# Kernel tuning notes

Hardware: AMD Instinct MI355X
Metric: run time of the kernel (lower is better)

## Reference

```python
import jax, jax.numpy as jnp
import numpy as np
import math

# Config (matches init_kwargs)
V, D, L, H, KVH, FF = 4054, 1024, 8, 16, 8, 4096
HD = D // H            # 64
NREP = H // KVH        # 2
THETA = 500000.0
EPS = 1e-5
PAD = 4053
B, S = 2, 2048


def setup_inputs() -> dict:
    key = jax.random.key(0)
    ks = jax.random.split(key, 12)
    std = 0.02
    inp = {
        "input_ids": jax.random.randint(ks[0], (B, S), 0, 4050),
        "emb": jax.random.normal(ks[1], (V, D), jnp.float32) * std,
        # Linear weights stored as [in, out] so y = x @ W
        "Wq": jax.random.normal(ks[2], (L, D, H * HD), jnp.float32) * std,
        "Wk": jax.random.normal(ks[3], (L, D, KVH * HD), jnp.float32) * std,
        "Wv": jax.random.normal(ks[4], (L, D, KVH * HD), jnp.float32) * std,
        "Wo": jax.random.normal(ks[5], (L, H * HD, D), jnp.float32) * std,
        "Wg": jax.random.normal(ks[6], (L, D, FF), jnp.float32) * std,
        "Wu": jax.random.normal(ks[7], (L, D, FF), jnp.float32) * std,
        "Wd": jax.random.normal(ks[8], (L, FF, D), jnp.float32) * std,
        "attn_norm_w": jnp.ones((L, D), jnp.float32),
        "ffn_norm_w": jnp.ones((L, D), jnp.float32),
        "final_norm_w": jnp.ones((D,), jnp.float32),
        "lm_head": jax.random.normal(ks[9], (D, V), jnp.float32) * std,
    }
    return inp


def _rms_norm(x, w):
    return x * jax.lax.rsqrt(jnp.mean(x * x, axis=-1, keepdims=True) + EPS) * w


def _rotate_half(x):
    x1, x2 = jnp.split(x, 2, axis=-1)
    return jnp.concatenate([-x2, x1], axis=-1)


def _rope_tables(seq_len):
    inv_freq = 1.0 / (THETA ** (jnp.arange(0, HD, 2, dtype=jnp.float32) / HD))
    t = jnp.arange(seq_len, dtype=jnp.float32)
    freqs = jnp.outer(t, inv_freq)            # [S, HD/2]
    ang = jnp.concatenate([freqs, freqs], -1)  # [S, HD]
    return jnp.cos(ang)[None, None], jnp.sin(ang)[None, None]  # [1,1,S,HD]


def reference(input_ids, emb, Wq, Wk, Wv, Wo, Wg, Wu, Wd,
              attn_norm_w, ffn_norm_w, final_norm_w, lm_head):
    b, s = input_ids.shape
    x = emb[input_ids]                                    # [B,S,D]

    cos, sin = _rope_tables(s)

    # causal mask + pad-key mask (pad tokens cannot be attended to)
    causal = jnp.triu(jnp.full((s, s), -jnp.inf, jnp.float32), k=1)
    pad_bias = jnp.where(input_ids == PAD, -jnp.inf, 0.0)  # [B,S]
    mask = causal[None, None] + pad_bias[:, None, None, :]  # [B,1,S,S]

    scale = 1.0 / math.sqrt(HD)

    def block(h, p):
        wq, wk, wv, wo, wg, wu, wd, anw, fnw = p
        hn = _rms_norm(h, anw)
        q = (hn @ wq).reshape(b, s, H, HD).transpose(0, 2, 1, 3)    # [B,H,S,hd]
        k = (hn @ wk).reshape(b, s, KVH, HD).transpose(0, 2, 1, 3)  # [B,KVH,S,hd]
        v = (hn @ wv).reshape(b, s, KVH, HD).transpose(0, 2, 1, 3)
        q = q * cos + _rotate_half(q) * sin
        k = k * cos + _rotate_half(k) * sin
        k = jnp.repeat(k, NREP, axis=1)  # GQA expand -> [B,H,S,hd]
        v = jnp.repeat(v, NREP, axis=1)
        scores = jnp.einsum('bhqd,bhkd->bhqk', q, k) * scale + mask  # fp32
        attn = jax.nn.softmax(scores, axis=-1)
        o = jnp.einsum('bhqk,bhkd->bhqd', attn, v)
        o = o.transpose(0, 2, 1, 3).reshape(b, s, H * HD)
        h = h + o @ wo
        hn = _rms_norm(h, fnw)
        h = h + (jax.nn.silu(hn @ wg) * (hn @ wu)) @ wd
        return h, None

    x, _ = jax.lax.scan(block, x, (Wq, Wk, Wv, Wo, Wg, Wu, Wd, attn_norm_w, ffn_norm_w))
    logits = _rms_norm(x, final_norm_w) @ lm_head          # [B,S,V]
    return logits
```

## Files before the change

kernel.cpp:

```cpp
#include <hip/hip_runtime.h>

constexpr int C_NTOK = 4096;
constexpr int C_DIM  = 1024;
constexpr int C_NL   = 8;
constexpr int C_NH   = 16;
constexpr int C_NKVH = 8;
constexpr int C_FF   = 4096;
constexpr int C_HD   = 64;
constexpr int C_B    = 2;
constexpr int C_S    = 2048;
constexpr int C_V    = 4054;
constexpr int C_PAD  = 4053;

typedef unsigned short u16;
typedef unsigned int   u32;
typedef __attribute__((ext_vector_type(4))) float f32x4;
typedef __attribute__((ext_vector_type(8))) short s16x8;

__device__ __forceinline__ float bf2f(u16 u) {
  u32 i = ((u32)u) << 16; float f; __builtin_memcpy(&f, &i, 4); return f;
}
__device__ __forceinline__ u16 f2bf(float f) {
  u32 i; __builtin_memcpy(&i, &f, 4);
  return (u16)((i + 0x7FFFu + ((i >> 16) & 1u)) >> 16);
}
__device__ __forceinline__ f32x4 mfma16(s16x8 a, s16x8 b, f32x4 c) {
  return __builtin_amdgcn_mfma_f32_16x16x32_bf16(a, b, c, 0, 0, 0);
}
__device__ __forceinline__ void gld16(const void* g, void* l) {
  __builtin_amdgcn_global_load_lds((const __attribute__((address_space(1))) unsigned int*)g,
                                   (__attribute__((address_space(3))) unsigned int*)l, 16, 0, 0);
}

__global__ __launch_bounds__(256) void k_embed(const int* __restrict__ ids,
                                               const float* __restrict__ emb,
                                               float* __restrict__ x) {
  int t = blockIdx.x;
  const float4* src = (const float4*)(emb + (size_t)ids[t] * C_DIM);
  float4* dst = (float4*)(x + (size_t)t * C_DIM);
  dst[threadIdx.x] = src[threadIdx.x];
}

__global__ void k_bias(const int* __restrict__ ids, float* __restrict__ bias) {
  int i = blockIdx.x * 256 + threadIdx.x;
  if (i < C_NTOK) bias[i] = (ids[i] == C_PAD) ? -1e30f : 0.0f;
}

__global__ __launch_bounds__(256) void k_rmsnorm(const float* __restrict__ x,
                                                 const float* __restrict__ w,
                                                 u16* __restrict__ out) {
  int row = blockIdx.x, tid = threadIdx.x;
  float4 v = ((const float4*)(x + (size_t)row * C_DIM))[tid];
  float ss = v.x * v.x + v.y * v.y + v.z * v.z + v.w * v.w;
#pragma unroll
  for (int d = 1; d < 64; d <<= 1) ss += __shfl_xor(ss, d, 64);
  __shared__ float sm[4];
  if ((tid & 63) == 0) sm[tid >> 6] = ss;
  __syncthreads();
  float tot = sm[0] + sm[1] + sm[2] + sm[3];
  float rs = 1.0f / sqrtf(tot * (1.0f / C_DIM) + 1e-5f);
  float4 wv = ((const float4*)w)[tid];
  uint2 o;
  o.x = (u32)f2bf(v.x * rs * wv.x) | ((u32)f2bf(v.y * rs * wv.y) << 16);
  o.y = (u32)f2bf(v.z * rs * wv.z) | ((u32)f2bf(v.w * rs * wv.w) << 16);
  ((uint2*)(out + (size_t)row * C_DIM))[tid] = o;
}

__global__ __launch_bounds__(256) void k_wT(const float* __restrict__ W,
                                            u16* __restrict__ Wt,
                                            int K, int N, size_t szW, size_t szWt) {
  __shared__ u16 T[64][72];
  W  += (size_t)blockIdx.z * szW;
  Wt += (size_t)blockIdx.z * szWt;
  const int n0 = blockIdx.x * 64, k0 = blockIdx.y * 64;
  const int tid = threadIdx.x;
  const int r = tid >> 4, c4 = (tid & 15) * 4;
  const bool vec = ((N & 3) == 0);
#pragma unroll
  for (int it = 0; it < 4; ++it) {
    int k = k0 + r + it * 16;
    int n = n0 + c4;
    float4 v;
    if (vec && (n + 3 < N)) {
      v = *(const float4*)&W[(size_t)k * N + n];
    } else {
      v.x = (n + 0 < N) ? W[(size_t)k * N + n + 0] : 0.f;
      v.y = (n + 1 < N) ? W[(size_t)k * N + n + 1] : 0.f;
      v.z = (n + 2 < N) ? W[(size_t)k * N + n + 2] : 0.f;
      v.w = (n + 3 < N) ? W[(size_t)k * N + n + 3] : 0.f;
    }
    T[c4 + 0][r + it * 16] = f2bf(v.x);
    T[c4 + 1][r + it * 16] = f2bf(v.y);
    T[c4 + 2][r + it * 16] = f2bf(v.z);
    T[c4 + 3][r + it * 16] = f2bf(v.w);
  }
  __syncthreads();
  const int rr = tid >> 3, cc = (tid & 7) * 8;
#pragma unroll
  for (int jt = 0; jt < 2; ++jt) {
    int n = rr + jt * 32;
    *(uint4*)&Wt[(size_t)(n0 + n) * K + k0 + cc] = *(const uint4*)&T[n][cc];
  }
}

template <int EPI, int NS>
__global__ __launch_bounds__(256) void k_gemm(const u16* __restrict__ A,
                                              const u16* __restrict__ Bt,
                                              void* __restrict__ Cp,
                                              int N, int K, int lda) {
  __shared__ u16 As[2][128 * 32];
  __shared__ u16 Bs[2][128 * 32];
  const int nx = gridDim.x;
  int lin = blockIdx.y * nx + blockIdx.x;
  const int nwg = nx * gridDim.y;
  if ((nwg & 7) == 0) lin = (lin & 7) * (nwg >> 3) + (lin >> 3);
  const int bm = (lin / nx) * 128, bn = (lin % nx) * 128;
  const int tid = threadIdx.x;
  const int lane = tid & 63, wid = tid >> 6;
  const int wr = wid >> 1, wc = wid & 1;
  const int l16 = lane & 15, lg = lane >> 4;
  const int srow = tid >> 2, scol = (tid & 3) * 8;
  const u16* Ab = A + (size_t)(bm + srow) * lda + scol;
  const u16* Bb = Bt + (size_t)(bn + srow) * K + scol;
  const int kchunk = K / NS;
  const int kb0 = blockIdx.z * kchunk, kb1 = kb0 + kchunk;
  f32x4 acc[4][4] = {};
  {
    u16* ad = &As[0][tid * 8];
    u16* bd = &Bs[0][tid * 8];
    gld16(Ab + kb0, ad);
    gld16(Ab + (size_t)64 * lda + kb0, ad + 2048);
    gld16(Bb + kb0, bd);
    gld16(Bb + (size_t)64 * K + kb0, bd + 2048);
  }
  __syncthreads();
  int cur = 0;
  for (int kb = kb0; kb < kb1; kb += 32) {
    const int nkb = kb + 32;
    if (nkb < kb1) {
      u16* ad = &As[cur ^ 1][tid * 8];
      u16* bd = &Bs[cur ^ 1][tid * 8];
      gld16(Ab + nkb, ad);
      gld16(Ab + (size_t)64 * lda + nkb, ad + 2048);
      gld16(Bb + nkb, bd);
      gld16(Bb + (size_t)64 * K + nkb, bd + 2048);
    }
    s16x8 af[4], bfr[4];
#pragma unroll
    for (int i = 0; i < 4; ++i)
      af[i] = *(const s16x8*)&As[cur][(64 * wr + 16 * i + l16) * 32 + 8 * lg];
#pragma unroll
    for (int i = 0; i < 4; ++i)
      bfr[i] = *(const s16x8*)&Bs[cur][(64 * wc + 16 * i + l16) * 32 + 8 * lg];
#pragma unroll
    for (int mi = 0; mi < 4; ++mi)
#pragma unroll
      for (int ni = 0; ni < 4; ++ni)
        acc[mi][ni] = mfma16(af[mi], bfr[ni], acc[mi][ni]);
    __syncthreads();
    cur ^= 1;
  }
#pragma unroll
  for (int mi = 0; mi < 4; ++mi)
#pragma unroll
    for (int ni = 0; ni < 4; ++ni)
#pragma unroll
      for (int r = 0; r < 4; ++r) {
        int row = bm + 64 * wr + 16 * mi + 4 * lg + r;
        int col = bn + 64 * wc + 16 * ni + l16;
        if (col >= N) continue;
        float val = acc[mi][ni][r];
        size_t off = (size_t)row * N + col;
        if (EPI == 0)      ((u16*)Cp)[off] = f2bf(val);
        else if (EPI == 1) ((float*)Cp)[off] = val;
        else if (NS == 1)  ((float*)Cp)[off] += val;
        else               unsafeAtomicAdd((float*)Cp + off, val);
      }
}

template <int EPI>
__global__ __launch_bounds__(512, 2) void k_gemm256(const u16* __restrict__ A,
                                                    const u16* __restrict__ Bt,
                                                    void* __restrict__ Cp,
                                                    int N, int K, int lda, int Nst) {
  __shared__ u16 As[2][16384];
  __shared__ u16 Bs[2][16384];
  const int nx = gridDim.x;
  int lin = blockIdx.y * nx + blockIdx.x;
  const int nwg = nx * gridDim.y;
  if ((nwg & 7) == 0) lin = (lin & 7) * (nwg >> 3) + (lin >> 3);
  const int bm = (lin / nx) * 256, bn = (lin % nx) * 256;
  const int tid = threadIdx.x;
  const int lane = tid & 63, wid = tid >> 6;
  const int wr = wid >> 2, wc = wid & 3;
  const int l16 = lane & 15, lg = lane >> 4;
  const int srow = tid >> 3;
  const int scol = (((tid & 7) ^ ((tid >> 3) & 7)) << 3);
  const u16* Ab = A + (size_t)(bm + srow) * lda + scol;
  const u16* Bb = Bt + (size_t)(bn + srow) * K + scol;
  const int NT = K >> 6;
  f32x4 acc[8][4] = {};

#define STG_A(b, i, kt) gld16(Ab + (size_t)((i) * 64) * lda + (kt), &As[b][(i) * 4096 + tid * 8])
#define STG_B(b, i, kt) gld16(Bb + (size_t)((i) * 64) * K + (kt), &Bs[b][(i) * 4096 + tid * 8])
#define STG_HALF(b, h, kt)                                     \
  do {                                                         \
    if ((h) == 0)      { STG_A(b, 0, kt); STG_A(b, 1, kt); }   \
    else if ((h) == 1) { STG_A(b, 2, kt); STG_A(b, 3, kt); }   \
    else if ((h) == 2) { STG_B(b, 0, kt); STG_B(b, 1, kt); }   \
    else               { STG_B(b, 2, kt); STG_B(b, 3, kt); }   \
  } while (0)
#define RD_FRAG(arr, b, row, kh)                                                     \
  (*(const s16x8*)((const char*)&arr[b][0] +                                         \
                   (((row) << 7) + (((((kh) << 2) + lg) ^ ((row) & 7)) << 4))))

  STG_HALF(0, 0, 0); STG_HALF(0, 1, 0); STG_HALF(0, 2, 0); STG_HALF(0, 3, 0);
  int c = 0;
  for (int j = 0; j < NT; ++j) {
    const int ktn = (j + 1) << 6;
    const bool pf = (j + 1 < NT);
    s16x8 af[4][2], bfr[4][2];
    if (pf) { STG_HALF(c ^ 1, 0, ktn); asm volatile("s_waitcnt vmcnt(2)" ::: "memory"); }
    else    { asm volatile("s_waitcnt vmcnt(0)" ::: "memory"); }
    __builtin_amdgcn_s_barrier();
    __builtin_amdgcn_sched_barrier(0);
#pragma unroll
    for (int i = 0; i < 4; ++i) {
      int row = wr * 128 + i * 16 + l16;
      af[i][0] = RD_FRAG(As, c, row, 0);
      af[i][1] = RD_FRAG(As, c, row, 1);
    }
#pragma unroll
    for (int n = 0; n < 2; ++n) {
      int row = wc * 64 + n * 16 + l16;
      bfr[n][0] = RD_FRAG(Bs, c, row, 0);
      bfr[n][1] = RD_FRAG(Bs, c, row, 1);
    }
    asm volatile("s_waitcnt lgkmcnt(0)" ::: "memory");
    __builtin_amdgcn_sched_barrier(0);
    __builtin_amdgcn_s_setprio(1);
#pragma unroll
    for (int i = 0; i < 4; ++i)
#pragma unroll
      for (int n = 0; n < 2; ++n) {
        acc[i][n] = mfma16(af[i][0], bfr[n][0], acc[i][n]);
        acc[i][n] = mfma16(af[i][1], bfr[n][1], acc[i][n]);
      }
    __builtin_amdgcn_s_setprio(0);
    __builtin_amdgcn_s_barrier();
#pragma unroll
    for (int n = 0; n < 2; ++n) {
      int row = wc * 64 + (2 + n) * 16 + l16;
      bfr[2 + n][0] = RD_FRAG(Bs, c, row, 0);
      bfr[2 + n][1] = RD_FRAG(Bs, c, row, 1);
    }
    if (pf) STG_HALF(c ^ 1, 1, ktn);
    __builtin_amdgcn_s_barrier();
    asm volatile("s_waitcnt lgkmcnt(0)" ::: "memory");
    __builtin_amdgcn_sched_barrier(0);
    __builtin_amdgcn_s_setprio(1);
#pragma unroll
    for (int i = 0; i < 4; ++i)
#pragma unroll
      for (int n = 0; n < 2; ++n) {
        acc[i][2 + n] = mfma16(af[i][0], bfr[2 + n][0], acc[i][2 + n]);
        acc[i][2 + n] = mfma16(af[i][1], bfr[2 + n][1], acc[i][2 + n]);
      }
    __builtin_amdgcn_s_setprio(0);
    __builtin_amdgcn_s_barrier();
#pragma unroll
    for (int i = 0; i < 4; ++i) {
      int row = wr * 128 + (4 + i) * 16 + l16;
      af[i][0] = RD_FRAG(As, c, row, 0);
      af[i][1] = RD_FRAG(As, c, row, 1);
    }
    if (pf) STG_HALF(c ^ 1, 2, ktn);
    __builtin_amdgcn_s_barrier();
    asm volatile("s_waitcnt lgkmcnt(0)" ::: "memory");
    __builtin_amdgcn_sched_barrier(0);
    __builtin_amdgcn_s_setprio(1);
#pragma unroll
    for (int i = 0; i < 4; ++i)
#pragma unroll
      for (int n = 0; n < 2; ++n) {
        acc[4 + i][n] = mfma16(af[i][0], bfr[n][0], acc[4 + i][n]);
        acc[4 + i][n] = mfma16(af[i][1], bfr[n][1], acc[4 + i][n]);
      }
    __builtin_amdgcn_s_setprio(0);
    __builtin_amdgcn_s_barrier();
    if (pf) STG_HALF(c ^ 1, 3, ktn);
    __builtin_amdgcn_s_barrier();
    __builtin_amdgcn_s_setprio(1);
#pragma unroll
    for (int i = 0; i < 4; ++i)
#pragma unroll
      for (int n = 0; n < 2; ++n) {
        acc[4 + i][2 + n] = mfma16(af[i][0], bfr[2 + n][0], acc[4 + i][2 + n]);
        acc[4 + i][2 + n] = mfma16(af[i][1], bfr[2 + n][1], acc[4 + i][2 + n]);
      }
    __builtin_amdgcn_s_setprio(0);
    __builtin_amdgcn_s_barrier();
    c ^= 1;
  }
#undef STG_A
#undef STG_B
#undef STG_HALF
#undef RD_FRAG
#pragma unroll
  for (int mi = 0; mi < 8; ++mi)
#pragma unroll
    for (int ni = 0; ni < 4; ++ni)
#pragma unroll
      for (int r = 0; r < 4; ++r) {
        int row = bm + wr * 128 + mi * 16 + 4 * lg + r;
        int col = bn + wc * 64 + ni * 16 + l16;
        float val = acc[mi][ni][r];
        if (EPI == 0) {
          ((u16*)Cp)[(size_t)row * N + col] = f2bf(val);
        } else {
          if (col < Nst) ((float*)Cp)[(size_t)row * Nst + col] = val;
        }
      }
}

__global__ void k_rope(u16* __restrict__ buf) {
  int idx = blockIdx.x * 256 + threadIdx.x;
  int j = idx & 15;
  int h = (idx >> 4) % 24;
  int t = idx / (16 * 24);
  int pos = t & (C_S - 1);
  const float L = 13.122363377404328f;
  float inv0 = expf(-(float)(4 * j)     * (1.0f / C_HD) * L);
  float inv1 = expf(-(float)(4 * j + 2) * (1.0f / C_HD) * L);
  float a0 = (float)pos * inv0, a1 = (float)pos * inv1;
  float c0 = cosf(a0), s0 = sinf(a0), c1 = cosf(a1), s1 = sinf(a1);
  int hoff = (h < 16) ? h * C_HD : 1024 + (h - 16) * C_HD;
  u16* pp = buf + (size_t)t * 2048 + hoff + 2 * j;
  u32 lo = *(u32*)pp;
  u32 hi = *(u32*)(pp + 32);
  float x0a = bf2f((u16)lo), x0b = bf2f((u16)(lo >> 16));
  float x1a = bf2f((u16)hi), x1b = bf2f((u16)(hi >> 16));
  *(u32*)pp        = (u32)f2bf(x0a * c0 - x1a * s0) | ((u32)f2bf(x0b * c1 - x1b * s1) << 16);
  *(u32*)(pp + 32) = (u32)f2bf(x1a * c0 + x0a * s0) | ((u32)f2bf(x1b * c1 + x0b * s1) << 16);
}

__global__ __launch_bounds__(256) void k_vT(const u16* __restrict__ qkv, u16* __restrict__ vt) {
  __shared__ u16 T[64][72];
  const int s0 = blockIdx.x * 64, kvh = blockIdx.y, b = blockIdx.z;
  const int tid = threadIdx.x;
  {
    const int r = tid >> 2, q = tid & 3;
    const u16* src = qkv + ((size_t)(b * C_S + s0 + r)) * 2048 + 1536 + kvh * C_HD + 16 * q;
    *(uint4*)&T[r][16 * q]     = *(const uint4*)src;
    *(uint4*)&T[r][16 * q + 8] = *(const uint4*)(src + 8);
  }
  __syncthreads();
  {
    const int hd = tid >> 2, sc4 = (tid & 3) * 16;
    u16 tmp[16];
#pragma unroll
    for (int jj = 0; jj < 16; ++jj) tmp[jj] = T[sc4 + jj][hd];
    u16* dst = vt + ((size_t)((b * C_NKVH + kvh) * C_HD + hd)) * C_S + s0 + sc4;
    *(uint4*)dst       = ((uint4*)tmp)[0];
    *(uint4*)(dst + 8) = ((uint4*)tmp)[1];
  }
}

__global__ __launch_bounds__(256) void k_pack(const u16* __restrict__ qkv,
                                              const u16* __restrict__ vt,
                                              u16* __restrict__ KP,
                                              u16* __restrict__ VP) {
  const int t = blockIdx.x, kvh = blockIdx.y, b = blockIdx.z;
  const int tid = threadIdx.x;
  const int lane = tid & 63, i4 = tid >> 6;
  const int l16 = lane & 15, lg = lane >> 4;
  const size_t obase = (((size_t)((b * 8 + kvh) * 32 + t)) * 8) * 512 + (size_t)lane * 8;
#pragma unroll
  for (int r = 0; r < 2; ++r) {
    int inst = i4 + 4 * r;
    int jt = inst >> 1, h = inst & 1;
    const u16* ks = qkv + (size_t)(b * C_S + 64 * t + 16 * jt + l16) * 2048
                    + 1024 + kvh * C_HD + 32 * h + 8 * lg;
    *(uint4*)(KP + obase + (size_t)inst * 512) = *(const uint4*)ks;
    const u16* vs = vt + ((size_t)((b * C_NKVH + kvh) * C_HD) + 16 * jt + l16) * C_S
                    + 64 * t + 32 * h + 8 * lg;
    *(uint4*)(VP + obase + (size_t)inst * 512) = *(const uint4*)vs;
  }
}

__global__ __launch_bounds__(64) void k_attn(const u16* __restrict__ qkv,
                                             const u16* __restrict__ KP,
                                             const u16* __restrict__ VP,
                                             const float* __restrict__ bias,
                                             u16* __restrict__ o) {
  const int qp = blockIdx.x, h = blockIdx.y, b = blockIdx.z;
  const int kvh = h >> 1;
  const int lane = threadIdx.x;
  const int l16 = lane & 15, lg = lane >> 4;
  __shared__ u16 P[16][72];
  const float* biasb = bias + b * C_S;
  const u16* kpb = KP + ((size_t)((b * 8 + kvh) * 32) * 8) * 512 + (size_t)lane * 8;
  const u16* vpb = VP + ((size_t)((b * 8 + kvh) * 32) * 8) * 512 + (size_t)lane * 8;
#pragma unroll
  for (int half = 0; half < 2; ++half) {
    const int qt = half ? (127 - qp) : qp;
    const int q0 = qt * 16;
    const int qrow = q0 + l16;
    const u16* qbase = qkv + (size_t)(b * C_S + qrow) * 2048 + h * C_HD + 8 * lg;
    s16x8 qf0 = *(const s16x8*)qbase;
    s16x8 qf1 = *(const s16x8*)(qbase + 32);
    float m = -1e30f, lsum = 0.f;
    f32x4 accO[4];
#pragma unroll
    for (int f = 0; f < 4; ++f) accO[f] = (f32x4){0.f, 0.f, 0.f, 0.f};
    const int nt = (q0 + 16 + 63) >> 6;
    s16x8 kf[8], vf[8];
#pragma unroll
    for (int i = 0; i < 8; ++i) kf[i] = *(const s16x8*)(kpb + (size_t)i * 512);
#pragma unroll
    for (int i = 0; i < 8; ++i) vf[i] = *(const s16x8*)(vpb + (size_t)i * 512);
    for (int t = 0; t < nt; ++t) {
      const int kt = t * 64;
      f32x4 sc[4];
#pragma unroll
      for (int jt = 0; jt < 4; ++jt) sc[jt] = (f32x4){0.f, 0.f, 0.f, 0.f};
#pragma unroll
      for (int jt = 0; jt < 4; ++jt) {
        sc[jt] = mfma16(kf[2 * jt],     qf0, sc[jt]);
        sc[jt] = mfma16(kf[2 * jt + 1], qf1, sc[jt]);
      }
      if (t + 1 < nt) {
        const u16* kn = kpb + (size_t)(t + 1) * 8 * 512;
#pragma unroll
        for (int i = 0; i < 8; ++i) kf[i] = *(const s16x8*)(kn + (size_t)i * 512);
      }
      float mt = -1e30f;
#pragma unroll
      for (int jt = 0; jt < 4; ++jt) {
        float4 bb = *(const float4*)&biasb[kt + 16 * jt + 4 * lg];
        int kv0 = kt + 16 * jt + 4 * lg;
        const float* bp = (const float*)&bb;
#pragma unroll
        for (int r = 0; r < 4; ++r) {
          float val = sc[jt][r] * 0.125f + bp[r];
          if (kv0 + r > qrow) val = -1e30f;
          sc[jt][r] = val;
          mt = fmaxf(mt, val);
        }
      }
      mt = fmaxf(mt, __shfl_xor(mt, 16, 64));
      mt = fmaxf(mt, __shfl_xor(mt, 32, 64));
      float mn = fmaxf(m, mt);
      float cc = __expf(m - mn);
      m = mn;
      float ps = 0.f;
#pragma unroll
      for (int jt = 0; jt < 4; ++jt)
#pragma unroll
        for (int r = 0; r < 4; ++r) {
          float pv = __expf(sc[jt][r] - m);
          sc[jt][r] = pv;
          ps += pv;
        }
      ps += __shfl_xor(ps, 16, 64);
      ps += __shfl_xor(ps, 32, 64);
      lsum = lsum * cc + ps;
#pragma unroll
      for (int f = 0; f < 4; ++f)
#pragma unroll
        for (int r = 0; r < 4; ++r) accO[f][r] *= cc;
#pragma unroll
      for (int jt = 0; jt < 4; ++jt) {
        uint2 w;
        w.x = (u32)f2bf(sc[jt][0]) | ((u32)f2bf(sc[jt][1]) << 16);
        w.y = (u32)f2bf(sc[jt][2]) | ((u32)f2bf(sc[jt][3]) << 16);
        *(uint2*)&P[l16][16 * jt + 4 * lg] = w;
      }
      asm volatile("s_waitcnt lgkmcnt(0)" ::: "memory");
      __builtin_amdgcn_sched_barrier(0);
      s16x8 pf0 = *(const s16x8*)&P[l16][8 * lg];
      s16x8 pf1 = *(const s16x8*)&P[l16][32 + 8 * lg];
#pragma unroll
      for (int f = 0; f < 4; ++f) {
        accO[f] = mfma16(vf[2 * f],     pf0, accO[f]);
        accO[f] = mfma16(vf[2 * f + 1], pf1, accO[f]);
      }
      if (t + 1 < nt) {
        const u16* vn = vpb + (size_t)(t + 1) * 8 * 512;
#pragma unroll
        for (int i = 0; i < 8; ++i) vf[i] = *(const s16x8*)(vn + (size_t)i * 512);
      }
    }
    float linv = 1.0f / lsum;
    u16* ob = o + ((size_t)(b * C_S + qrow)) * 1024 + h * C_HD + 4 * lg;
#pragma unroll
    for (int f = 0; f < 4; ++f) {
      uint2 w;
      w.x = (u32)f2bf(accO[f][0] * linv) | ((u32)f2bf(accO[f][1] * linv) << 16);
      w.y = (u32)f2bf(accO[f][2] * linv) | ((u32)f2bf(accO[f][3] * linv) << 16);
      *(uint2*)(ob + 16 * f) = w;
    }
  }
}

__global__ void k_silumul(u16* __restrict__ gu) {
  int idx = blockIdx.x * 256 + threadIdx.x;
  int row = idx >> 9;
  int c8 = (idx & 511) * 8;
  u16* g = gu + (size_t)row * 8192 + c8;
  const u16* u = g + 4096;
  uint4 gv = *(const uint4*)g;
  uint4 uv = *(const uint4*)u;
  u32* gp = (u32*)&gv;
  u32* up = (u32*)&uv;
  u32 go[4];
#pragma unroll
  for (int j = 0; j < 4; ++j) {
    float g0 = bf2f((u16)(gp[j] & 0xffff)), g1 = bf2f((u16)(gp[j] >> 16));
    float u0 = bf2f((u16)(up[j] & 0xffff)), u1 = bf2f((u16)(up[j] >> 16));
    float s0 = g0 / (1.0f + __expf(-g0));
    float s1 = g1 / (1.0f + __expf(-g1));
    go[j] = (u32)f2bf(s0 * u0) | ((u32)f2bf(s1 * u1) << 16);
  }
  *(uint4*)g = *(uint4*)go;
}

extern "C" void kernel_launch(void* const* d_in, const int* in_sizes, int n_in,
                              void* d_out, int out_size, void* d_ws, size_t ws_size,
                              hipStream_t stream) {
  const int*   ids  = (const int*)d_in[0];
  const float* emb  = (const float*)d_in[1];
  const float* Wq   = (const float*)d_in[2];
  const float* Wk   = (const float*)d_in[3];
  const float* Wv   = (const float*)d_in[4];
  const float* Wo   = (const float*)d_in[5];
  const float* Wg   = (const float*)d_in[6];
  const float* Wu   = (const float*)d_in[7];
  const float* Wd   = (const float*)d_in[8];
  const float* anw  = (const float*)d_in[9];
  const float* fnw  = (const float*)d_in[10];
  const float* finw = (const float*)d_in[11];
  const float* lmh  = (const float*)d_in[12];

  char* p = (char*)d_ws;
  float* x  = (float*)p; p += (size_t)C_NTOK * C_DIM * 4;
  u16* hn   = (u16*)p;   p += (size_t)C_NTOK * C_DIM * 2;
  u16* qkv  = (u16*)p;   p += (size_t)C_NTOK * 2048 * 2;
  u16* vtb  = (u16*)p;   p += (size_t)C_NTOK * C_NKVH * C_HD * 2;
  u16* ao   = (u16*)p;   p += (size_t)C_NTOK * C_NH * C_HD * 2;
  u16* gu   = (u16*)p;   p += (size_t)C_NTOK * 2 * C_FF * 2;
  u16* wT   = (u16*)p;   p += (size_t)8192 * 1024 * 2;
  float* bias = (float*)p; p += (size_t)C_NTOK * 4;
  u16* KP   = (u16*)p;   p += (size_t)C_B * 8 * 32 * 8 * 512 * 2;
  u16* VP   = (u16*)p;   p += (size_t)C_B * 8 * 32 * 8 * 512 * 2;
  u16* wTall = (u16*)p;

  const size_t M1 = 1024 * 1024;
  const size_t O_qkv = 0;
  const size_t O_wo  = O_qkv + 16 * M1;
  const size_t O_gu  = O_wo + 8 * M1;
  const size_t O_wd  = O_gu + 64 * M1;
  const size_t O_lmh = O_wd + 32 * M1;
  const size_t wTall_elems = O_lmh + 4 * M1;
  const size_t needed = ((char*)wTall - (char*)d_ws) + wTall_elems * 2;
  const bool big = ws_size >= needed;

  k_embed<<<C_NTOK, 256, 0, stream>>>(ids, emb, x);
  k_bias<<<C_NTOK / 256, 256, 0, stream>>>(ids, bias);

  if (big) {
    k_wT<<<dim3(16, 16, 8), 256, 0, stream>>>(Wq, wTall + O_qkv, C_DIM, 1024, M1, 2 * M1);
    k_wT<<<dim3(8, 16, 8), 256, 0, stream>>>(Wk, wTall + O_qkv + M1, C_DIM, 512, M1 / 2, 2 * M1);
    k_wT<<<dim3(8, 16, 8), 256, 0, stream>>>(Wv, wTall + O_qkv + M1 + M1 / 2, C_DIM, 512, M1 / 2, 2 * M1);
    k_wT<<<dim3(16, 16, 8), 256, 0, stream>>>(Wo, wTall + O_wo, 1024, C_DIM, M1, M1);
    k_wT<<<dim3(64, 16, 8), 256, 0, stream>>>(Wg, wTall + O_gu, C_DIM, C_FF, 4 * M1, 8 * M1);
    k_wT<<<dim3(64, 16, 8), 256, 0, stream>>>(Wu, wTall + O_gu + 4 * M1, C_DIM, C_FF, 4 * M1, 8 * M1);
    k_wT<<<dim3(16, 64, 8), 256, 0, stream>>>(Wd, wTall + O_wd, C_FF, C_DIM, 4 * M1, 4 * M1);
    k_wT<<<dim3(64, 16, 1), 256, 0, stream>>>(lmh, wTall + O_lmh, C_DIM, C_V, 0, 0);
  }

  for (int l = 0; l < C_NL; ++l) {
    k_rmsnorm<<<C_NTOK, 256, 0, stream>>>(x, anw + (size_t)l * C_DIM, hn);
    const u16* qkvT;
    if (big) {
      qkvT = wTall + O_qkv + (size_t)l * 2 * M1;
    } else {
      k_wT<<<dim3(16, 16), 256, 0, stream>>>(Wq + (size_t)l * M1, wT, C_DIM, 1024, 0, 0);
      k_wT<<<dim3(8, 16), 256, 0, stream>>>(Wk + (size_t)l * M1 / 2, wT + M1, C_DIM, 512, 0, 0);
      k_wT<<<dim3(8, 16), 256, 0, stream>>>(Wv + (size_t)l * M1 / 2, wT + M1 + M1 / 2, C_DIM, 512, 0, 0);
      qkvT = wT;
    }
    k_gemm<0, 1><<<dim3(16, 32), 256, 0, stream>>>(hn, qkvT, qkv, 2048, C_DIM, C_DIM);
    k_rope<<<C_NTOK * 24 * 16 / 256, 256, 0, stream>>>(qkv);
    k_vT<<<dim3(C_S / 64, C_NKVH, C_B), 256, 0, stream>>>(qkv, vtb);
    k_pack<<<dim3(32, C_NKVH, C_B), 256, 0, stream>>>(qkv, vtb, KP, VP);
    k_attn<<<dim3(64, C_NH, C_B), 64, 0, stream>>>(qkv, KP, VP, bias, ao);
    const u16* woT;
    if (big) {
      woT = wTall + O_wo + (size_t)l * M1;
    } else {
      k_wT<<<dim3(16, 16), 256, 0, stream>>>(Wo + (size_t)l * M1, wT, 1024, C_DIM, 0, 0);
      woT = wT;
    }
    k_gemm<2, 2><<<dim3(8, 32, 2), 256, 0, stream>>>(ao, woT, x, C_DIM, 1024, 1024);
    k_rmsnorm<<<C_NTOK, 256, 0, stream>>>(x, fnw + (size_t)l * C_DIM, hn);
    const u16* guT;
    if (big) {
      guT = wTall + O_gu + (size_t)l * 8 * M1;
    } else {
      k_wT<<<dim3(64, 16), 256, 0, stream>>>(Wg + (size_t)l * 4 * M1, wT, C_DIM, C_FF, 0, 0);
      k_wT<<<dim3(64, 16), 256, 0, stream>>>(Wu + (size_t)l * 4 * M1, wT + 4 * M1, C_DIM, C_FF, 0, 0);
      guT = wT;
    }
    k_gemm256<0><<<dim3(32, 16), 512, 0, stream>>>(hn, guT, gu, 8192, C_DIM, C_DIM, 8192);
    k_silumul<<<C_NTOK * 512 / 256, 256, 0, stream>>>(gu);
    const u16* wdT;
    if (big) {
      wdT = wTall + O_wd + (size_t)l * 4 * M1;
    } else {
      k_wT<<<dim3(16, 64), 256, 0, stream>>>(Wd + (size_t)l * 4 * M1, wT, C_FF, C_DIM, 0, 0);
      wdT = wT;
    }
    k_gemm<2, 4><<<dim3(8, 32, 4), 256, 0, stream>>>(gu, wdT, x, C_DIM, C_FF, 8192);
  }
  k_rmsnorm<<<C_NTOK, 256, 0, stream>>>(x, finw, hn);
  const u16* lmhT;
  if (big) {
    lmhT = wTall + O_lmh;
  } else {
    k_wT<<<dim3(64, 16), 256, 0, stream>>>(lmh, wT, C_DIM, C_V, 0, 0);
    lmhT = wT;
  }
  k_gemm256<1><<<dim3(16, 16), 512, 0, stream>>>(hn, lmhT, d_out, 4096, C_DIM, C_DIM, C_V);
}
```

Before: 2.915 ms.

## Fuse SiLU-mul into gate/up GEMM epilogue and V transpose into pack

Gate and up weight columns are interleaved in 128-column chunks so each 256-wide GEMM tile holds matching gate and up halves. The epilogue swaps halves through LDS and writes silu(g)*u directly, which removes the separate silumul pass and halves the intermediate buffer write. Separately, the V transpose kernel is merged into the pack kernel through an LDS tile, saving one launch and a round trip through global memory. The cost is an extra LDS exchange and a synchronisation in the GEMM epilogue.

Result: faster. 2.843 ms (-2.5%).

```diff
diff --git a/kernel.cpp b/kernel.cpp
--- a/kernel.cpp
+++ b/kernel.cpp
@@ -68,11 +68,13 @@
 
 __global__ __launch_bounds__(256) void k_wT(const float* __restrict__ W,
                                             u16* __restrict__ Wt,
-                                            int K, int N, size_t szW, size_t szWt) {
+                                            int K, int N, size_t szW, size_t szWt,
+                                            int ilv) {
   __shared__ u16 T[64][72];
   W  += (size_t)blockIdx.z * szW;
   Wt += (size_t)blockIdx.z * szWt;
   const int n0 = blockIdx.x * 64, k0 = blockIdx.y * 64;
+  const int dbase = (ilv < 0) ? n0 : (((n0 >> 7) << 8) + (n0 & 127) + ilv);
   const int tid = threadIdx.x;
   const int r = tid >> 4, c4 = (tid & 15) * 4;
   const bool vec = ((N & 3) == 0);
@@ -99,7 +101,7 @@
 #pragma unroll
   for (int jt = 0; jt < 2; ++jt) {
     int n = rr + jt * 32;
-    *(uint4*)&Wt[(size_t)(n0 + n) * K + k0 + cc] = *(const uint4*)&T[n][cc];
+    *(uint4*)&Wt[(size_t)(dbase + n) * K + k0 + cc] = *(const uint4*)&T[n][cc];
   }
 }
 
@@ -306,6 +308,37 @@
 #undef STG_B
 #undef STG_HALF
 #undef RD_FRAG
+  if (EPI == 2) {
+    if (wc >= 2) {
+      const int cc2 = wc - 2;
+      float* dst = (wr == 0) ? (float*)&As[0][0] : (float*)&Bs[0][0];
+#pragma unroll
+      for (int mi = 0; mi < 8; ++mi)
+#pragma unroll
+        for (int ni = 0; ni < 4; ++ni)
+#pragma unroll
+          for (int r = 0; r < 4; ++r)
+            dst[(((cc2 << 7) + (mi * 16 + 4 * lg + r)) << 6) + ni * 16 + l16] = acc[mi][ni][r];
+    }
+    __syncthreads();
+    if (wc < 2) {
+      const float* src = (wr == 0) ? (const float*)&As[0][0] : (const float*)&Bs[0][0];
+#pragma unroll
+      for (int mi = 0; mi < 8; ++mi)
+#pragma unroll
+        for (int ni = 0; ni < 4; ++ni)
+#pragma unroll
+          for (int r = 0; r < 4; ++r) {
+            float g = acc[mi][ni][r];
+            float u = src[(((wc << 7) + (mi * 16 + 4 * lg + r)) << 6) + ni * 16 + l16];
+            float s = g / (1.0f + __expf(-g));
+            int row = bm + wr * 128 + mi * 16 + 4 * lg + r;
+            int col = (bn >> 1) + wc * 64 + ni * 16 + l16;
+            ((u16*)Cp)[(size_t)row * Nst + col] = f2bf(s * u);
+          }
+    }
+    return;
+  }
 #pragma unroll
   for (int mi = 0; mi < 8; ++mi)
 #pragma unroll
@@ -344,34 +377,19 @@
   *(u32*)(pp + 32) = (u32)f2bf(x1a * c0 + x0a * s0) | ((u32)f2bf(x1b * c1 + x0b * s1) << 16);
 }
 
-__global__ __launch_bounds__(256) void k_vT(const u16* __restrict__ qkv, u16* __restrict__ vt) {
-  __shared__ u16 T[64][72];
-  const int s0 = blockIdx.x * 64, kvh = blockIdx.y, b = blockIdx.z;
-  const int tid = threadIdx.x;
-  {
-    const int r = tid >> 2, q = tid & 3;
-    const u16* src = qkv + ((size_t)(b * C_S + s0 + r)) * 2048 + 1536 + kvh * C_HD + 16 * q;
-    *(uint4*)&T[r][16 * q]     = *(const uint4*)src;
-    *(uint4*)&T[r][16 * q + 8] = *(const uint4*)(src + 8);
-  }
-  __syncthreads();
-  {
-    const int hd = tid >> 2, sc4 = (tid & 3) * 16;
-    u16 tmp[16];
-#pragma unroll
-    for (int jj = 0; jj < 16; ++jj) tmp[jj] = T[sc4 + jj][hd];
-    u16* dst = vt + ((size_t)((b * C_NKVH + kvh) * C_HD + hd)) * C_S + s0 + sc4;
-    *(uint4*)dst       = ((uint4*)tmp)[0];
-    *(uint4*)(dst + 8) = ((uint4*)tmp)[1];
-  }
-}
-
 __global__ __launch_bounds__(256) void k_pack(const u16* __restrict__ qkv,
-                                              const u16* __restrict__ vt,
                                               u16* __restrict__ KP,
                                               u16* __restrict__ VP) {
   const int t = blockIdx.x, kvh = blockIdx.y, b = blockIdx.z;
   const int tid = threadIdx.x;
+  __shared__ u16 T[64][72];
+  {
+    const int r = tid >> 2, q = tid & 3;
+    const u16* src = qkv + ((size_t)(b * C_S + 64 * t + r)) * 2048 + 1536 + kvh * C_HD + 16 * q;
+    *(uint4*)&T[r][16 * q]     = *(const uint4*)src;
+    *(uint4*)&T[r][16 * q + 8] = *(const uint4*)(src + 8);
+  }
+  __syncthreads();
   const int lane = tid & 63, i4 = tid >> 6;
   const int l16 = lane & 15, lg = lane >> 4;
   const size_t obase = (((size_t)((b * 8 + kvh) * 32 + t)) * 8) * 512 + (size_t)lane * 8;
@@ -382,9 +400,10 @@
     const u16* ks = qkv + (size_t)(b * C_S + 64 * t + 16 * jt + l16) * 2048
                     + 1024 + kvh * C_HD + 32 * h + 8 * lg;
     *(uint4*)(KP + obase + (size_t)inst * 512) = *(const uint4*)ks;
-    const u16* vs = vt + ((size_t)((b * C_NKVH + kvh) * C_HD) + 16 * jt + l16) * C_S
-                    + 64 * t + 32 * h + 8 * lg;
-    *(uint4*)(VP + obase + (size_t)inst * 512) = *(const uint4*)vs;
+    u16 vtmp[8];
+#pragma unroll
+    for (int j = 0; j < 8; ++j) vtmp[j] = T[32 * h + 8 * lg + j][16 * jt + l16];
+    *(uint4*)(VP + obase + (size_t)inst * 512) = *(uint4*)vtmp;
   }
 }
 
@@ -501,28 +520,6 @@
       *(uint2*)(ob + 16 * f) = w;
     }
   }
-}
-
-__global__ void k_silumul(u16* __restrict__ gu) {
-  int idx = blockIdx.x * 256 + threadIdx.x;
-  int row = idx >> 9;
-  int c8 = (idx & 511) * 8;
-  u16* g = gu + (size_t)row * 8192 + c8;
-  const u16* u = g + 4096;
-  uint4 gv = *(const uint4*)g;
-  uint4 uv = *(const uint4*)u;
-  u32* gp = (u32*)&gv;
-  u32* up = (u32*)&uv;
-  u32 go[4];
-#pragma unroll
-  for (int j = 0; j < 4; ++j) {
-    float g0 = bf2f((u16)(gp[j] & 0xffff)), g1 = bf2f((u16)(gp[j] >> 16));
-    float u0 = bf2f((u16)(up[j] & 0xffff)), u1 = bf2f((u16)(up[j] >> 16));
-    float s0 = g0 / (1.0f + __expf(-g0));
-    float s1 = g1 / (1.0f + __expf(-g1));
-    go[j] = (u32)f2bf(s0 * u0) | ((u32)f2bf(s1 * u1) << 16);
-  }
-  *(uint4*)g = *(uint4*)go;
 }
 
 extern "C" void kernel_launch(void* const* d_in, const int* in_sizes, int n_in,
@@ -554,6 +551,7 @@
   u16* KP   = (u16*)p;   p += (size_t)C_B * 8 * 32 * 8 * 512 * 2;
   u16* VP   = (u16*)p;   p += (size_t)C_B * 8 * 32 * 8 * 512 * 2;
   u16* wTall = (u16*)p;
+  (void)vtb;
 
   const size_t M1 = 1024 * 1024;
   const size_t O_qkv = 0;
@@ -569,14 +567,14 @@
   k_bias<<<C_NTOK / 256, 256, 0, stream>>>(ids, bias);
 
   if (big) {
-    k_wT<<<dim3(16, 16, 8), 256, 0, stream>>>(Wq, wTall + O_qkv, C_DIM, 1024, M1, 2 * M1);
-    k_wT<<<dim3(8, 16, 8), 256, 0, stream>>>(Wk, wTall + O_qkv + M1, C_DIM, 512, M1 / 2, 2 * M1);
-    k_wT<<<dim3(8, 16, 8), 256, 0, stream>>>(Wv, wTall + O_qkv + M1 + M1 / 2, C_DIM, 512, M1 / 2, 2 * M1);
-    k_wT<<<dim3(16, 16, 8), 256, 0, stream>>>(Wo, wTall + O_wo, 1024, C_DIM, M1, M1);
-    k_wT<<<dim3(64, 16, 8), 256, 0, stream>>>(Wg, wTall + O_gu, C_DIM, C_FF, 4 * M1, 8 * M1);
-    k_wT<<<dim3(64, 16, 8), 256, 0, stream>>>(Wu, wTall + O_gu + 4 * M1, C_DIM, C_FF, 4 * M1, 8 * M1);
-    k_wT<<<dim3(16, 64, 8), 256, 0, stream>>>(Wd, wTall + O_wd, C_FF, C_DIM, 4 * M1, 4 * M1);
-    k_wT<<<dim3(64, 16, 1), 256, 0, stream>>>(lmh, wTall + O_lmh, C_DIM, C_V, 0, 0);
+    k_wT<<<dim3(16, 16, 8), 256, 0, stream>>>(Wq, wTall + O_qkv, C_DIM, 1024, M1, 2 * M1, -1);
+    k_wT<<<dim3(8, 16, 8), 256, 0, stream>>>(Wk, wTall + O_qkv + M1, C_DIM, 512, M1 / 2, 2 * M1, -1);
+    k_wT<<<dim3(8, 16, 8), 256, 0, stream>>>(Wv, wTall + O_qkv + M1 + M1 / 2, C_DIM, 512, M1 / 2, 2 * M1, -1);
+    k_wT<<<dim3(16, 16, 8), 256, 0, stream>>>(Wo, wTall + O_wo, 1024, C_DIM, M1, M1, -1);
+    k_wT<<<dim3(64, 16, 8), 256, 0, stream>>>(Wg, wTall + O_gu, C_DIM, C_FF, 4 * M1, 8 * M1, 0);
+    k_wT<<<dim3(64, 16, 8), 256, 0, stream>>>(Wu, wTall + O_gu, C_DIM, C_FF, 4 * M1, 8 * M1, 128);
+    k_wT<<<dim3(16, 64, 8), 256, 0, stream>>>(Wd, wTall + O_wd, C_FF, C_DIM, 4 * M1, 4 * M1, -1);
+    k_wT<<<dim3(64, 16, 1), 256, 0, stream>>>(lmh, wTall + O_lmh, C_DIM, C_V, 0, 0, -1);
   }
 
   for (int l = 0; l < C_NL; ++l) {
@@ -585,21 +583,20 @@
     if (big) {
       qkvT = wTall + O_qkv + (size_t)l * 2 * M1;
     } else {
-      k_wT<<<dim3(16, 16), 256, 0, stream>>>(Wq + (size_t)l * M1, wT, C_DIM, 1024, 0, 0);
-      k_wT<<<dim3(8, 16), 256, 0, stream>>>(Wk + (size_t)l * M1 / 2, wT + M1, C_DIM, 512, 0, 0);
-      k_wT<<<dim3(8, 16), 256, 0, stream>>>(Wv + (size_t)l * M1 / 2, wT + M1 + M1 / 2, C_DIM, 512, 0, 0);
+      k_wT<<<dim3(16, 16), 256, 0, stream>>>(Wq + (size_t)l * M1, wT, C_DIM, 1024, 0, 0, -1);
+      k_wT<<<dim3(8, 16), 256, 0, stream>>>(Wk + (size_t)l * M1 / 2, wT + M1, C_DIM, 512, 0, 0, -1);
+      k_wT<<<dim3(8, 16), 256, 0, stream>>>(Wv + (size_t)l * M1 / 2, wT + M1 + M1 / 2, C_DIM, 512, 0, 0, -1);
       qkvT = wT;
     }
     k_gemm<0, 1><<<dim3(16, 32), 256, 0, stream>>>(hn, qkvT, qkv, 2048, C_DIM, C_DIM);
     k_rope<<<C_NTOK * 24 * 16 / 256, 256, 0, stream>>>(qkv);
-    k_vT<<<dim3(C_S / 64, C_NKVH, C_B), 256, 0, stream>>>(qkv, vtb);
-    k_pack<<<dim3(32, C_NKVH, C_B), 256, 0, stream>>>(qkv, vtb, KP, VP);
+    k_pack<<<dim3(32, C_NKVH, C_B), 256, 0, stream>>>(qkv, KP, VP);
     k_attn<<<dim3(64, C_NH, C_B), 64, 0, stream>>>(qkv, KP, VP, bias, ao);
     const u16* woT;
     if (big) {
       woT = wTall + O_wo + (size_t)l * M1;
     } else {
-      k_wT<<<dim3(16, 16), 256, 0, stream>>>(Wo + (size_t)l * M1, wT, 1024, C_DIM, 0, 0);
+      k_wT<<<dim3(16, 16), 256, 0, stream>>>(Wo + (size_t)l * M1, wT, 1024, C_DIM, 0, 0, -1);
       woT = wT;
     }
     k_gemm<2, 2><<<dim3(8, 32, 2), 256, 0, stream>>>(ao, woT, x, C_DIM, 1024, 1024);
@@ -608,27 +605,26 @@
     if (big) {
       guT = wTall + O_gu + (size_t)l * 8 * M1;
     } else {
-      k_wT<<<dim3(64, 16), 256, 0, stream>>>(Wg + (size_t)l * 4 * M1, wT, C_DIM, C_FF, 0, 0);
-      k_wT<<<dim3(64, 16), 256, 0, stream>>>(Wu + (size_t)l * 4 * M1, wT + 4 * M1, C_DIM, C_FF, 0, 0);
+      k_wT<<<dim3(64, 16), 256, 0, stream>>>(Wg + (size_t)l * 4 * M1, wT, C_DIM, C_FF, 0, 0, 0);
+      k_wT<<<dim3(64, 16), 256, 0, stream>>>(Wu + (size_t)l * 4 * M1, wT, C_DIM, C_FF, 0, 0, 128);
       guT = wT;
     }
-    k_gemm256<0><<<dim3(32, 16), 512, 0, stream>>>(hn, guT, gu, 8192, C_DIM, C_DIM, 8192);
-    k_silumul<<<C_NTOK * 512 / 256, 256, 0, stream>>>(gu);
+    k_gemm256<2><<<dim3(32, 16), 512, 0, stream>>>(hn, guT, gu, 8192, C_DIM, C_DIM, 4096);
     const u16* wdT;
     if (big) {
       wdT = wTall + O_wd + (size_t)l * 4 * M1;
     } else {
-      k_wT<<<dim3(16, 64), 256, 0, stream>>>(Wd + (size_t)l * 4 * M1, wT, C_FF, C_DIM, 0, 0);
+      k_wT<<<dim3(16, 64), 256, 0, stream>>>(Wd + (size_t)l * 4 * M1, wT, C_FF, C_DIM, 0, 0, -1);
       wdT = wT;
     }
-    k_gemm<2, 4><<<dim3(8, 32, 4), 256, 0, stream>>>(gu, wdT, x, C_DIM, C_FF, 8192);
+    k_gemm<2, 4><<<dim3(8, 32, 4), 256, 0, stream>>>(gu, wdT, x, C_DIM, C_FF, 4096);
   }
   k_rmsnorm<<<C_NTOK, 256, 0, stream>>>(x, finw, hn);
   const u16* lmhT;
   if (big) {
     lmhT = wTall + O_lmh;
   } else {
-    k_wT<<<dim3(64, 16), 256, 0, stream>>>(lmh, wT, C_DIM, C_V, 0, 0);
+    k_wT<<<dim3(64, 16), 256, 0, stream>>>(lmh, wT, C_DIM, C_V, 0, 0, -1);
     lmhT = wT;
   }
   k_gemm256<1><<<dim3(16, 16), 512, 0, stream>>>(hn, lmhT, d_out, 4096, C_DIM, C_DIM, C_V);
```
